# Kernel tuning notes

Measured on AMD Instinct MI355X. Metric: run time of the kernel, lower is better.

## Reference

```python
import jax, jax.numpy as jnp
import numpy as np

B, N, C, K = 2, 4096, 256, 64


def setup_inputs() -> dict:
    key = jax.random.key(0)
    k1, k2, k3, k4, k5, k6 = jax.random.split(key, 6)
    points = jax.random.normal(k1, (B, N, 3), dtype=jnp.float32)  # ~N(0,1) cloud
    point_features = jax.random.normal(k2, (B, N, C), dtype=jnp.float32)
    # proposals: centers inside the cloud, positive box dims, random yaw (unused by mask math)
    centers = jax.random.uniform(k3, (B, K, 3), minval=-1.0, maxval=1.0, dtype=jnp.float32)
    dims = jax.random.uniform(k4, (B, K, 3), minval=0.5, maxval=1.5, dtype=jnp.float32)
    ry = jax.random.uniform(k5, (B, K, 1), minval=-np.pi, maxval=np.pi, dtype=jnp.float32)
    proposals = jnp.concatenate([centers, dims, ry], axis=-1)  # (B,K,7)
    W1 = jax.random.normal(k6, (C, 256), dtype=jnp.float32) * (1.0 / np.sqrt(C))
    b1 = jnp.zeros((256,), dtype=jnp.float32)
    W2 = jax.random.normal(jax.random.fold_in(key, 7), (256, 256), dtype=jnp.float32) * (1.0 / 16.0)
    b2 = jnp.zeros((256,), dtype=jnp.float32)
    return {"points": points, "point_features": point_features, "proposals": proposals,
            "W1": W1, "b1": b1, "W2": W2, "b2": b2}


def reference(points, point_features, proposals, W1, b1, W2, b2):
    # points: (B,N,3), point_features: (B,N,C), proposals: (B,K,7)
    ctr = proposals[..., :3]                      # (B,K,3) cx,cy,cz
    half = proposals[..., 3:6] * 0.5              # (B,K,3) l/2,w/2,h/2
    lo = ctr - half                               # (B,K,3)
    hi = ctr + half
    # point-in-box mask (axis-aligned, strict inequalities as in source): (B,K,N)
    p = points[:, None, :, :]                     # (B,1,N,3)
    mask = jnp.all((p > lo[:, :, None, :]) & (p < hi[:, :, None, :]), axis=-1)
    any_in = jnp.any(mask, axis=-1)               # (B,K)
    # masked max-pool over points: (B,K,N,C) -> (B,K,C)
    neg_inf = jnp.asarray(-jnp.inf, point_features.dtype)
    masked = jnp.where(mask[..., None], point_features[:, None, :, :], neg_inf)
    pooled = jnp.max(masked, axis=2)
    pooled = jnp.where(any_in[..., None], pooled, 0.0)  # empty box -> zeros
    # fc: Linear(C,256) + ReLU + Linear(256,256) + ReLU
    h = jax.nn.relu(jnp.einsum('bkc,cd->bkd', pooled, W1) + b1)
    out = jax.nn.relu(jnp.einsum('bkd,de->bke', h, W2) + b2)
    return out
```

## Files before the change

kernel.cpp:

```cpp
#include <hip/hip_runtime.h>

#define Bn 2
#define Nn 4096
#define Cn 256
#define Kn 64
#define BK (Bn * Kn)
#define NT 1024
#define NG 4
#define CG (Cn / NG)

__global__ __launch_bounds__(NT) void roi_onepass_kernel(
    const float* __restrict__ points,
    const float* __restrict__ feats,
    const float* __restrict__ proposals,
    const float* __restrict__ W1,
    const float* __restrict__ b1,
    const float* __restrict__ W2,
    const float* __restrict__ b2,
    float* __restrict__ out)
{
    const int bk   = blockIdx.x;
    const int b    = bk / Kn;
    const int tid  = threadIdx.x;
    const int lane = tid & (Cn - 1);
    const int grp  = tid >> 8;

    __shared__ int   s_idx[Nn];
    __shared__ int   s_count;
    __shared__ float s_red[NG][Cn];
    __shared__ float s_vec[Cn];

    const float* prop = proposals + (size_t)bk * 7;
    const float cx = prop[0], cy = prop[1], cz = prop[2];
    const float hx = prop[3] * 0.5f, hy = prop[4] * 0.5f, hz = prop[5] * 0.5f;
    const float lox = cx - hx, loy = cy - hy, loz = cz - hz;
    const float hix = cx + hx, hiy = cy + hy, hiz = cz + hz;

    if (tid == 0) s_count = 0;
    __syncthreads();

    const float* pts = points + (size_t)b * Nn * 3;
    #pragma unroll
    for (int n = tid; n < Nn; n += NT) {
        const float px = pts[n * 3 + 0];
        const float py = pts[n * 3 + 1];
        const float pz = pts[n * 3 + 2];
        const bool in = (px > lox) & (px < hix) &
                        (py > loy) & (py < hiy) &
                        (pz > loz) & (pz < hiz);
        if (in) s_idx[atomicAdd(&s_count, 1)] = n;
    }
    __syncthreads();
    const int count = s_count;

    const int i0 = (count * grp)       / NG;
    const int i1 = (count * (grp + 1)) / NG;
    const float* fb = feats + (size_t)b * Nn * Cn + lane;

    float m = -INFINITY;
    int i = i0;
    for (; i + 8 <= i1; i += 8) {
        const int a0 = s_idx[i + 0], a1 = s_idx[i + 1];
        const int a2 = s_idx[i + 2], a3 = s_idx[i + 3];
        const int a4 = s_idx[i + 4], a5 = s_idx[i + 5];
        const int a6 = s_idx[i + 6], a7 = s_idx[i + 7];
        const float f0 = fb[(size_t)a0 * Cn];
        const float f1 = fb[(size_t)a1 * Cn];
        const float f2 = fb[(size_t)a2 * Cn];
        const float f3 = fb[(size_t)a3 * Cn];
        const float f4 = fb[(size_t)a4 * Cn];
        const float f5 = fb[(size_t)a5 * Cn];
        const float f6 = fb[(size_t)a6 * Cn];
        const float f7 = fb[(size_t)a7 * Cn];
        m = fmaxf(m, fmaxf(fmaxf(fmaxf(f0, f1), fmaxf(f2, f3)),
                           fmaxf(fmaxf(f4, f5), fmaxf(f6, f7))));
    }
    for (; i < i1; ++i) m = fmaxf(m, fb[(size_t)s_idx[i] * Cn]);

    s_red[grp][lane] = m;
    __syncthreads();

    float mm = fmaxf(fmaxf(s_red[0][lane], s_red[1][lane]),
                     fmaxf(s_red[2][lane], s_red[3][lane]));
    if (count == 0) mm = 0.0f;
    if (grp == 0) s_vec[lane] = mm;
    __syncthreads();

    {
        const int c0 = grp * CG;
        float acc = 0.0f;
        #pragma unroll 16
        for (int j = 0; j < CG; ++j) {
            const int c = c0 + j;
            acc = fmaf(s_vec[c], W1[c * Cn + lane], acc);
        }
        s_red[grp][lane] = acc;
    }
    __syncthreads();
    const float h = fmaxf(s_red[0][lane] + s_red[1][lane] +
                          s_red[2][lane] + s_red[3][lane] + b1[lane], 0.0f);
    __syncthreads();
    if (grp == 0) s_vec[lane] = h;
    __syncthreads();

    {
        const int c0 = grp * CG;
        float acc = 0.0f;
        #pragma unroll 16
        for (int j = 0; j < CG; ++j) {
            const int c = c0 + j;
            acc = fmaf(s_vec[c], W2[c * Cn + lane], acc);
        }
        s_red[grp][lane] = acc;
    }
    __syncthreads();
    if (grp == 0) {
        const float o = fmaxf(s_red[0][lane] + s_red[1][lane] +
                              s_red[2][lane] + s_red[3][lane] + b2[lane], 0.0f);
        out[(size_t)bk * Cn + lane] = o;
    }
}

extern "C" void kernel_launch(void* const* d_in, const int* in_sizes, int n_in,
                              void* d_out, int out_size, void* d_ws, size_t ws_size,
                              hipStream_t stream) {
    const float* points    = (const float*)d_in[0];
    const float* feats     = (const float*)d_in[1];
    const float* proposals = (const float*)d_in[2];
    const float* W1        = (const float*)d_in[3];
    const float* b1        = (const float*)d_in[4];
    const float* W2        = (const float*)d_in[5];
    const float* b2        = (const float*)d_in[6];
    float* out             = (float*)d_out;

    roi_onepass_kernel<<<BK, NT, 0, stream>>>(points, feats, proposals,
                                              W1, b1, W2, b2, out);
}
```

Baseline: 92.40 us.

## Gather features as float4 per wave, ballot-compact indices, two-level max reduce

Point compaction now uses one wave-level ballot and a single atomic per wavefront instead of one atomic per point. The masked max-pool is rewritten so each of 16 waves takes a contiguous slice of the in-box points and reads whole 1 KB feature rows with float4 loads, keeping 16 independent loads in flight with clamped tail indices. The partial maxima are then combined through a two-stage shared-memory reduction. This is meant to cut memory instruction count and raise memory-level parallelism, at the cost of more registers, some redundant loads at the tail and an extra barrier.

```diff
diff --git a/kernel.cpp b/kernel.cpp
--- a/kernel.cpp
+++ b/kernel.cpp
@@ -6,10 +6,14 @@
 #define Kn 64
 #define BK (Bn * Kn)
 #define NT 1024
-#define NG 4
-#define CG (Cn / NG)
+#define NW 16
 
-__global__ __launch_bounds__(NT) void roi_onepass_kernel(
+static __device__ __forceinline__ float4 fmax4(float4 a, float4 b) {
+    return make_float4(fmaxf(a.x, b.x), fmaxf(a.y, b.y),
+                       fmaxf(a.z, b.z), fmaxf(a.w, b.w));
+}
+
+__global__ __launch_bounds__(NT) void roi_onepass_v2(
     const float* __restrict__ points,
     const float* __restrict__ feats,
     const float* __restrict__ proposals,
@@ -22,12 +26,12 @@
     const int bk   = blockIdx.x;
     const int b    = bk / Kn;
     const int tid  = threadIdx.x;
-    const int lane = tid & (Cn - 1);
-    const int grp  = tid >> 8;
+    const int w    = tid >> 6;
+    const int l    = tid & 63;
 
-    __shared__ int   s_idx[Nn];
-    __shared__ int   s_count;
-    __shared__ float s_red[NG][Cn];
+    __shared__ int s_idx[Nn];
+    __shared__ int s_count;
+    __shared__ __align__(16) float s_red[NW][Cn];
     __shared__ float s_vec[Cn];
 
     const float* prop = proposals + (size_t)bk * 7;
@@ -48,49 +52,61 @@
         const bool in = (px > lox) & (px < hix) &
                         (py > loy) & (py < hiy) &
                         (pz > loz) & (pz < hiz);
-        if (in) s_idx[atomicAdd(&s_count, 1)] = n;
+        const unsigned long long mask = __ballot(in);
+        int base = 0;
+        if (l == 0) base = atomicAdd(&s_count, __popcll(mask));
+        base = __shfl(base, 0);
+        if (in) s_idx[base + __popcll(mask & ((1ull << l) - 1ull))] = n;
     }
     __syncthreads();
     const int count = s_count;
 
-    const int i0 = (count * grp)       / NG;
-    const int i1 = (count * (grp + 1)) / NG;
-    const float* fb = feats + (size_t)b * Nn * Cn + lane;
-
-    float m = -INFINITY;
-    int i = i0;
-    for (; i + 8 <= i1; i += 8) {
-        const int a0 = s_idx[i + 0], a1 = s_idx[i + 1];
-        const int a2 = s_idx[i + 2], a3 = s_idx[i + 3];
-        const int a4 = s_idx[i + 4], a5 = s_idx[i + 5];
-        const int a6 = s_idx[i + 6], a7 = s_idx[i + 7];
-        const float f0 = fb[(size_t)a0 * Cn];
-        const float f1 = fb[(size_t)a1 * Cn];
-        const float f2 = fb[(size_t)a2 * Cn];
-        const float f3 = fb[(size_t)a3 * Cn];
-        const float f4 = fb[(size_t)a4 * Cn];
-        const float f5 = fb[(size_t)a5 * Cn];
-        const float f6 = fb[(size_t)a6 * Cn];
-        const float f7 = fb[(size_t)a7 * Cn];
-        m = fmaxf(m, fmaxf(fmaxf(fmaxf(f0, f1), fmaxf(f2, f3)),
-                           fmaxf(fmaxf(f4, f5), fmaxf(f6, f7))));
+    float4 m4 = make_float4(-INFINITY, -INFINITY, -INFINITY, -INFINITY);
+    if (count > 0) {
+        const int cpw = (count + NW - 1) >> 4;
+        const int i0  = w * cpw;
+        const float4* fb4 = (const float4*)(feats + (size_t)b * Nn * Cn);
+        for (int i = i0; i < i0 + cpw; i += 16) {
+            float4 v[16];
+            #pragma unroll
+            for (int t = 0; t < 16; ++t) {
+                int j = i + t;
+                j = (j < count) ? j : (count - 1);
+                const int n = s_idx[j];
+                v[t] = fb4[(size_t)n * 64 + l];
+            }
+            #pragma unroll
+            for (int t = 0; t < 8; ++t) v[t] = fmax4(v[t], v[t + 8]);
+            #pragma unroll
+            for (int t = 0; t < 4; ++t) v[t] = fmax4(v[t], v[t + 4]);
+            v[0] = fmax4(fmax4(v[0], v[1]), fmax4(v[2], v[3]));
+            m4 = fmax4(m4, v[0]);
+        }
     }
-    for (; i < i1; ++i) m = fmaxf(m, fb[(size_t)s_idx[i] * Cn]);
-
-    s_red[grp][lane] = m;
-    __syncthreads();
-
-    float mm = fmaxf(fmaxf(s_red[0][lane], s_red[1][lane]),
-                     fmaxf(s_red[2][lane], s_red[3][lane]));
-    if (count == 0) mm = 0.0f;
-    if (grp == 0) s_vec[lane] = mm;
+    ((float4*)&s_red[w][0])[l] = m4;
     __syncthreads();
 
     {
-        const int c0 = grp * CG;
+        const int c = tid & 255, g = tid >> 8;
+        const float a = fmaxf(fmaxf(s_red[4 * g + 0][c], s_red[4 * g + 1][c]),
+                              fmaxf(s_red[4 * g + 2][c], s_red[4 * g + 3][c]));
+        s_red[4 * g][c] = a;
+    }
+    __syncthreads();
+    if (tid < 256) {
+        float mm = fmaxf(fmaxf(s_red[0][tid], s_red[4][tid]),
+                         fmaxf(s_red[8][tid], s_red[12][tid]));
+        if (count == 0) mm = 0.0f;
+        s_vec[tid] = mm;
+    }
+    __syncthreads();
+
+    const int grp = tid >> 8, lane = tid & 255;
+    {
+        const int c0 = grp * 64;
         float acc = 0.0f;
         #pragma unroll 16
-        for (int j = 0; j < CG; ++j) {
+        for (int j = 0; j < 64; ++j) {
             const int c = c0 + j;
             acc = fmaf(s_vec[c], W1[c * Cn + lane], acc);
         }
@@ -102,12 +118,11 @@
     __syncthreads();
     if (grp == 0) s_vec[lane] = h;
     __syncthreads();
-
     {
-        const int c0 = grp * CG;
+        const int c0 = grp * 64;
         float acc = 0.0f;
         #pragma unroll 16
-        for (int j = 0; j < CG; ++j) {
+        for (int j = 0; j < 64; ++j) {
             const int c = c0 + j;
             acc = fmaf(s_vec[c], W2[c * Cn + lane], acc);
         }
@@ -133,6 +148,6 @@
     const float* b2        = (const float*)d_in[6];
     float* out             = (float*)d_out;
 
-    roi_onepass_kernel<<<BK, NT, 0, stream>>>(points, feats, proposals,
-                                              W1, b1, W2, b2, out);
+    roi_onepass_v2<<<BK, NT, 0, stream>>>(points, feats, proposals,
+                                          W1, b1, W2, b2, out);
 }
```

After: 93.50 us. Within noise of the previous version (+1.2%).
